# Kernel optimization log

Hardware: AMD Instinct MI355X
Metric: run time of the kernel (lower is better)

Reference implementation:

```python
import jax, jax.numpy as jnp
import numpy as np

N, D, H, DEG = 20000, 128, 128, 32


def setup_inputs() -> dict:
    key = jax.random.key(0)
    ks = jax.random.split(key, 6)
    s = 0.02
    h = jax.random.normal(ks[0], (N, D), dtype=jnp.float32)
    # per-node neighbor indices, sorted by index (permutation invariance per docstring)
    nbr_idx = jnp.sort(jax.random.randint(ks[1], (N, DEG), 0, N), axis=-1)
    W_ih = jax.random.normal(ks[2], (4 * H, D), dtype=jnp.float32) * s
    W_hh = jax.random.normal(ks[3], (4 * H, H), dtype=jnp.float32) * s
    b_ih = jnp.zeros((4 * H,), jnp.float32)
    b_hh = jnp.zeros((4 * H,), jnp.float32)
    W_out = jax.random.normal(ks[4], (H, D + H), dtype=jnp.float32) * s
    b_out = jnp.zeros((H,), jnp.float32)
    return {"h": h, "nbr_idx": nbr_idx, "W_ih": W_ih, "W_hh": W_hh,
            "b_ih": b_ih, "b_hh": b_hh, "W_out": W_out, "b_out": b_out}


def reference(h, nbr_idx, W_ih, W_hh, b_ih, b_hh, W_out, b_out):
    # Gather neighbor features: [N, DEG, D]
    nbr = h[nbr_idx]
    # Precompute input-to-gate projections for all steps: [N, DEG, 4H]
    xg = jnp.einsum('ndi,gi->ndg', nbr, W_ih) + b_ih + b_hh
    xg = jnp.swapaxes(xg, 0, 1)  # [DEG, N, 4H] for scan over neighbor sequence
    h0 = jnp.zeros((h.shape[0], W_hh.shape[1]), h.dtype)
    c0 = jnp.zeros_like(h0)

    def step(carry, g_t):
        hp, cp = carry
        g = g_t + hp @ W_hh.T            # [N, 4H]
        i, f, gg, o = jnp.split(g, 4, axis=-1)  # PyTorch gate order i,f,g,o
        c = jax.nn.sigmoid(f) * cp + jax.nn.sigmoid(i) * jnp.tanh(gg)
        hn = jax.nn.sigmoid(o) * jnp.tanh(c)
        return (hn, c), None

    (agg, _), _ = jax.lax.scan(step, (h0, c0), xg)  # agg = final hidden state [N, H]
    combined = jnp.concatenate([h, agg], axis=-1)   # [N, D+H]
    return jax.nn.relu(combined @ W_out.T + b_out)  # [N, H]
```

## Files before the change

kernel.cpp:

```cpp
#include <hip/hip_runtime.h>

#define NN 20000
#define DD 128
#define HH 128
#define G4 512
#define DEG 32
#define NPB 48
#define NBLK 417

typedef __attribute__((ext_vector_type(4))) float f32x4;
typedef __attribute__((ext_vector_type(8))) short s16x8;

#ifndef __has_builtin
#define __has_builtin(x) 0
#endif

static __device__ __forceinline__ float fexp2(float x){
#if __has_builtin(__builtin_amdgcn_exp2f)
  return __builtin_amdgcn_exp2f(x);
#else
  return exp2f(x);
#endif
}
static __device__ __forceinline__ float frcp(float x){
#if __has_builtin(__builtin_amdgcn_rcpf)
  return __builtin_amdgcn_rcpf(x);
#else
  return 1.f/x;
#endif
}

static __device__ __forceinline__ unsigned cvt_pk_bf16(float lo, float hi){
  unsigned r;
  asm("v_cvt_pk_bf16_f32 %0, %1, %2" : "=v"(r) : "v"(lo), "v"(hi));
  return r;
}
static __device__ __forceinline__ s16x8 ld8bf(const float* __restrict__ p){
  f32x4 a = *(const f32x4*)p;
  f32x4 b = *(const f32x4*)(p+4);
  union{unsigned u[4]; s16x8 v;} z;
  z.u[0]=cvt_pk_bf16(a[0],a[1]);
  z.u[1]=cvt_pk_bf16(a[2],a[3]);
  z.u[2]=cvt_pk_bf16(b[0],b[1]);
  z.u[3]=cvt_pk_bf16(b[2],b[3]);
  return z.v;
}
static __device__ __forceinline__ s16x8 ld8bf_s(const float* __restrict__ p, float s){
  f32x4 a = *(const f32x4*)p;
  f32x4 b = *(const f32x4*)(p+4);
  union{unsigned u[4]; s16x8 v;} z;
  z.u[0]=cvt_pk_bf16(a[0]*s,a[1]*s);
  z.u[1]=cvt_pk_bf16(a[2]*s,a[3]*s);
  z.u[2]=cvt_pk_bf16(b[0]*s,b[1]*s);
  z.u[3]=cvt_pk_bf16(b[2]*s,b[3]*s);
  return z.v;
}
static __device__ __forceinline__ float lo16f(unsigned u){
  union{unsigned x; float f;} v; v.x = u << 16; return v.f;
}
static __device__ __forceinline__ float hi16f(unsigned u){
  union{unsigned x; float f;} v; v.x = u & 0xffff0000u; return v.f;
}
#define NLOG2E -1.44269504f
#define TLOG2E  2.88539008f

__global__ __launch_bounds__(512,2) void k_hp(
    const float* __restrict__ h, const float* __restrict__ W_ih,
    const float* __restrict__ b_ih, const float* __restrict__ b_hh,
    unsigned short* __restrict__ Hp)
{
  const int tid=threadIdx.x, w=tid>>6, lane=tid&63, lo=lane&15, hi=lane>>4;
  const float SC[4]={NLOG2E,NLOG2E,TLOG2E,NLOG2E};
  s16x8 A[4][4];
#pragma unroll
  for(int g=0;g<4;++g){
    const float* wr=W_ih+(size_t)(128*g+16*w+lo)*DD+8*hi;
#pragma unroll
    for(int c=0;c<4;++c) A[g][c]=ld8bf_s(wr+32*c, SC[g]);
  }
  f32x4 bb[4];
#pragma unroll
  for(int g=0;g<4;++g){
    const int gcb=128*g+16*w+4*hi;
    bb[g]=(*(const f32x4*)(b_ih+gcb) + *(const f32x4*)(b_hh+gcb))*SC[g];
  }
  const int nchunk = (blockIdx.x < 57) ? 2 : 1;
  for(int cc=0; cc<nchunk; ++cc){
    const int n0 = ((cc? 256+blockIdx.x : blockIdx.x))*64;
    f32x4 acc[4][4];
#pragma unroll
    for(int g=0;g<4;++g)
#pragma unroll
      for(int nt=0;nt<4;++nt) acc[g][nt]=(f32x4)0.f;
#pragma unroll
    for(int c=0;c<4;++c){
      s16x8 B[4];
#pragma unroll
      for(int nt=0;nt<4;++nt){
        int nd=n0+16*nt+lo; if(nd>=NN) nd=NN-1;
        B[nt]=ld8bf(h+(size_t)nd*DD+32*c+8*hi);
      }
#pragma unroll
      for(int g=0;g<4;++g)
#pragma unroll
        for(int nt=0;nt<4;++nt)
          acc[g][nt]=__builtin_amdgcn_mfma_f32_16x16x32_bf16(A[g][c],B[nt],acc[g][nt],0,0,0);
    }
#pragma unroll
    for(int nt=0;nt<4;++nt){
      int nd=n0+16*nt+lo;
      if(nd<NN){
        unsigned short* p = Hp + (size_t)nd*G4 + w*64 + hi*16;
        uint4 q0, q1;
        q0.x=cvt_pk_bf16(acc[0][nt][0]+bb[0][0], acc[0][nt][1]+bb[0][1]);
        q0.y=cvt_pk_bf16(acc[0][nt][2]+bb[0][2], acc[0][nt][3]+bb[0][3]);
        q0.z=cvt_pk_bf16(acc[1][nt][0]+bb[1][0], acc[1][nt][1]+bb[1][1]);
        q0.w=cvt_pk_bf16(acc[1][nt][2]+bb[1][2], acc[1][nt][3]+bb[1][3]);
        q1.x=cvt_pk_bf16(acc[2][nt][0]+bb[2][0], acc[2][nt][1]+bb[2][1]);
        q1.y=cvt_pk_bf16(acc[2][nt][2]+bb[2][2], acc[2][nt][3]+bb[2][3]);
        q1.z=cvt_pk_bf16(acc[3][nt][0]+bb[3][0], acc[3][nt][1]+bb[3][1]);
        q1.w=cvt_pk_bf16(acc[3][nt][2]+bb[3][2], acc[3][nt][3]+bb[3][3]);
        *(uint4*)p = q0;
        *(uint4*)(p+8) = q1;
      }
    }
  }
}

static __device__ __forceinline__ void unpack_acc(const uint4 q[2], f32x4 acc[4]){
  acc[0][0]=lo16f(q[0].x); acc[0][1]=hi16f(q[0].x); acc[0][2]=lo16f(q[0].y); acc[0][3]=hi16f(q[0].y);
  acc[1][0]=lo16f(q[0].z); acc[1][1]=hi16f(q[0].z); acc[1][2]=lo16f(q[0].w); acc[1][3]=hi16f(q[0].w);
  acc[2][0]=lo16f(q[1].x); acc[2][1]=hi16f(q[1].x); acc[2][2]=lo16f(q[1].y); acc[2][3]=hi16f(q[1].y);
  acc[3][0]=lo16f(q[1].z); acc[3][1]=hi16f(q[1].z); acc[3][2]=lo16f(q[1].w); acc[3][3]=hi16f(q[1].w);
}

static __device__ __forceinline__ void cell_update(const f32x4 acc[4], float C[4],
                                                   char* wb, int waddr){
  float hv[4];
#pragma unroll
  for(int r=0;r<4;++r){
    float ei=fexp2(acc[0][r]);
    float ef=fexp2(acc[1][r]);
    float eg=fexp2(acc[2][r]);
    float eo=fexp2(acc[3][r]);
    float itgT=__builtin_fmaf(eg, TLOG2E, -TLOG2E)*frcp((1.f+ei)*(1.f+eg));
    float Cn=__builtin_fmaf(C[r], frcp(1.f+ef), itgT);
    C[r]=Cn;
    float ec=fexp2(Cn);
    hv[r]=(ec-1.f)*frcp((1.f+eo)*(1.f+ec));
  }
  uint2 pk;
  pk.x=cvt_pk_bf16(hv[0],hv[1]);
  pk.y=cvt_pk_bf16(hv[2],hv[3]);
  *(uint2*)(wb + waddr) = pk;
}

__global__ __launch_bounds__(512,1) void k_lstm(
    const float* __restrict__ h, const int* __restrict__ nbr,
    const float* __restrict__ W_hh, const unsigned short* __restrict__ Hp,
    const float* __restrict__ W_out, const float* __restrict__ b_out,
    float* __restrict__ out)
{
  __shared__ unsigned short hpd[3][2][16*HH];
  __shared__ int nlds[DEG*NPB];
  const int tid=threadIdx.x, w=tid>>6, lane=tid&63, lo=lane&15, hi=lane>>4;
  const int n0=blockIdx.x*NPB;
  const int swz=(lo&7)<<4;
  const int woff=w*64+hi*16;
  const int waddr=((lo*256 + 32*w + 8*hi) ^ swz);
  const float SC[4]={NLOG2E,NLOG2E,TLOG2E,NLOG2E};

  s16x8 A[4][4];
#pragma unroll
  for(int g=0;g<4;++g){
    const float* wr=W_hh+(size_t)(128*g+16*w+lo)*HH+8*hi;
#pragma unroll
    for(int c=0;c<4;++c) A[g][c]=ld8bf_s(wr+32*c, SC[g]);
  }
  {
#pragma unroll
    for(int g=0;g<3;++g){
      unsigned* z=(unsigned*)&hpd[g][0][0];
      z[tid]=0u; z[tid+512]=0u;
    }
#pragma unroll
    for(int i=0;i<3;++i){
      int idx=tid+512*i;
      int node=idx>>5;
      int src=n0+node; if(src>=NN) src=NN-1;
      nlds[(idx&31)*NPB + node] = nbr[src*DEG + (idx&31)]*G4;
    }
  }
  __syncthreads();

  float cst[3][4]={{0.f,0.f,0.f,0.f},{0.f,0.f,0.f,0.f},{0.f,0.f,0.f,0.f}};

  uint4 qA[2], qB[2], qC[2];
  {
    const unsigned short* gp=Hp+(size_t)nlds[lo]+woff;
    qA[0]=*(const uint4*)gp; qA[1]=*(const uint4*)(gp+8);
  }

#define PHASE(g, QUSE, QLOAD, LOFF) { \
    { const unsigned short* gp_=Hp+(size_t)nlds[LOFF]+woff; \
      QLOAD[0]=*(const uint4*)gp_; QLOAD[1]=*(const uint4*)(gp_+8); } \
    s16x8 Bg[4]; \
    const char* rb_=(const char*)&hpd[g][t&1][0]; \
    _Pragma("unroll") \
    for(int c=0;c<4;++c) Bg[c]=*(const s16x8*)(rb_ + (((lo*256 + 64*c + 16*hi)) ^ swz)); \
    f32x4 acc_[4]; \
    unpack_acc(QUSE, acc_); \
    _Pragma("unroll") \
    for(int c=0;c<4;++c) \
      _Pragma("unroll") \
      for(int gg=0;gg<4;++gg) \
        acc_[gg]=__builtin_amdgcn_mfma_f32_16x16x32_bf16(A[gg][c],Bg[c],acc_[gg],0,0,0); \
    cell_update(acc_, cst[g], (char*)&hpd[g][(t+1)&1][0], waddr); }

  for(int t=0;t<DEG;++t){
    const int tn=(t+1<DEG)? t+1 : t;
    PHASE(0, qA, qB, t*NPB + 16 + lo)
    PHASE(1, qB, qC, t*NPB + 32 + lo)
    PHASE(2, qC, qA, tn*NPB + lo)
    asm volatile("s_waitcnt lgkmcnt(0)\n\ts_barrier" ::: "memory");
  }
#undef PHASE

  s16x8 AO[8];
  {
    const float* wr=W_out+(size_t)(16*w+lo)*256+8*hi;
#pragma unroll
    for(int c=0;c<8;++c) AO[c]=ld8bf(wr+32*c);
  }
  const int ob=16*w+4*hi;
  f32x4 bias=*(const f32x4*)(b_out+ob);
#pragma unroll
  for(int g=0;g<3;++g){
    const int node=n0+g*16+lo;
    const int nc = (node<NN)? node : NN-1;
    s16x8 BB[8];
    const float* hr=h+(size_t)nc*DD+8*hi;
#pragma unroll
    for(int c=0;c<4;++c) BB[c]=ld8bf(hr+32*c);
    const char* rb=(const char*)&hpd[g][0][0];
#pragma unroll
    for(int c=0;c<4;++c)
      BB[4+c]=*(const s16x8*)(rb + (((lo*256 + 64*c + 16*hi)) ^ swz));
    f32x4 acc=(f32x4)0.f;
#pragma unroll
    for(int c=0;c<8;++c) acc=__builtin_amdgcn_mfma_f32_16x16x32_bf16(AO[c],BB[c],acc,0,0,0);
#pragma unroll
    for(int r=0;r<4;++r){ float v=acc[r]+bias[r]; acc[r]=v>0.f?v:0.f; }
    if(node<NN) *(f32x4*)(out+(size_t)node*HH+ob)=acc;
  }
}

extern "C" void kernel_launch(void* const* d_in, const int* in_sizes, int n_in,
                              void* d_out, int out_size, void* d_ws, size_t ws_size,
                              hipStream_t stream)
{
  const float* h     = (const float*)d_in[0];
  const int*   nbr   = (const int*)d_in[1];
  const float* W_ih  = (const float*)d_in[2];
  const float* W_hh  = (const float*)d_in[3];
  const float* b_ih  = (const float*)d_in[4];
  const float* b_hh  = (const float*)d_in[5];
  const float* W_out = (const float*)d_in[6];
  const float* b_out = (const float*)d_in[7];
  unsigned short* Hp = (unsigned short*)d_ws;

  k_hp<<<256, 512, 0, stream>>>(h, W_ih, b_ih, b_hh, Hp);
  k_lstm<<<NBLK, 512, 0, stream>>>(h, nbr, W_hh, Hp, W_out, b_out, (float*)d_out);
}
```

Baseline: 212.0 us.

## Use persistent LSTM blocks with atomic work queue over 32-node tiles

The recurrence kernel now processes 32 nodes per tile (two 16-node groups) instead of 48, launches a fixed grid of 512 persistent blocks at two blocks per CU, and pulls further tiles from a global atomic counter that the first kernel resets. This aims to fix the tail imbalance of 417 one-shot blocks and raise occupancy so more waves hide latency. In exchange, each wave has less interleaving of independent recurrences to cover MFMA and gather latency, and each tile pays an extra barrier plus an atomic. The counter reset depends on the first kernel running before the second on the same stream.

```diff
diff --git a/kernel.cpp b/kernel.cpp
--- a/kernel.cpp
+++ b/kernel.cpp
@@ -5,8 +5,9 @@
 #define HH 128
 #define G4 512
 #define DEG 32
-#define NPB 48
-#define NBLK 417
+#define NPB 32
+#define PAIRS 625
+#define GRID2 512
 
 typedef __attribute__((ext_vector_type(4))) float f32x4;
 typedef __attribute__((ext_vector_type(8))) short s16x8;
@@ -14,6 +15,8 @@
 #ifndef __has_builtin
 #define __has_builtin(x) 0
 #endif
+
+__device__ int g_cnt;
 
 static __device__ __forceinline__ float fexp2(float x){
 #if __has_builtin(__builtin_amdgcn_exp2f)
@@ -69,6 +72,7 @@
     const float* __restrict__ b_ih, const float* __restrict__ b_hh,
     unsigned short* __restrict__ Hp)
 {
+  if(blockIdx.x==0 && threadIdx.x==0) g_cnt = GRID2;
   const int tid=threadIdx.x, w=tid>>6, lane=tid&63, lo=lane&15, hi=lane>>4;
   const float SC[4]={NLOG2E,NLOG2E,TLOG2E,NLOG2E};
   s16x8 A[4][4];
@@ -155,16 +159,16 @@
   *(uint2*)(wb + waddr) = pk;
 }
 
-__global__ __launch_bounds__(512,1) void k_lstm(
+__global__ __launch_bounds__(512,2) void k_lstm(
     const float* __restrict__ h, const int* __restrict__ nbr,
     const float* __restrict__ W_hh, const unsigned short* __restrict__ Hp,
     const float* __restrict__ W_out, const float* __restrict__ b_out,
     float* __restrict__ out)
 {
-  __shared__ unsigned short hpd[3][2][16*HH];
+  __shared__ unsigned short hpd[2][2][16*HH];
   __shared__ int nlds[DEG*NPB];
+  __shared__ int spair;
   const int tid=threadIdx.x, w=tid>>6, lane=tid&63, lo=lane&15, hi=lane>>4;
-  const int n0=blockIdx.x*NPB;
   const int swz=(lo&7)<<4;
   const int woff=w*64+hi*16;
   const int waddr=((lo*256 + 32*w + 8*hi) ^ swz);
@@ -177,29 +181,31 @@
 #pragma unroll
     for(int c=0;c<4;++c) A[g][c]=ld8bf_s(wr+32*c, SC[g]);
   }
-  {
-#pragma unroll
-    for(int g=0;g<3;++g){
-      unsigned* z=(unsigned*)&hpd[g][0][0];
-      z[tid]=0u; z[tid+512]=0u;
-    }
-#pragma unroll
-    for(int i=0;i<3;++i){
-      int idx=tid+512*i;
-      int node=idx>>5;
-      int src=n0+node; if(src>=NN) src=NN-1;
-      nlds[(idx&31)*NPB + node] = nbr[src*DEG + (idx&31)]*G4;
-    }
-  }
-  __syncthreads();
-
-  float cst[3][4]={{0.f,0.f,0.f,0.f},{0.f,0.f,0.f,0.f},{0.f,0.f,0.f,0.f}};
-
-  uint4 qA[2], qB[2], qC[2];
-  {
-    const unsigned short* gp=Hp+(size_t)nlds[lo]+woff;
-    qA[0]=*(const uint4*)gp; qA[1]=*(const uint4*)(gp+8);
-  }
+
+  int pair = blockIdx.x;
+  for(;;){
+    const int n0 = pair*NPB;
+    {
+#pragma unroll
+      for(int g=0;g<2;++g){
+        unsigned* z=(unsigned*)&hpd[g][0][0];
+        z[tid]=0u; z[tid+512]=0u;
+      }
+#pragma unroll
+      for(int i=0;i<2;++i){
+        int idx=tid+512*i;
+        nlds[(idx&31)*NPB + (idx>>5)] = nbr[n0*DEG + idx]*G4;
+      }
+    }
+    __syncthreads();
+
+    float cst[2][4]={{0.f,0.f,0.f,0.f},{0.f,0.f,0.f,0.f}};
+
+    uint4 qA[2], qB[2];
+    {
+      const unsigned short* gp=Hp+(size_t)nlds[lo]+woff;
+      qA[0]=*(const uint4*)gp; qA[1]=*(const uint4*)(gp+8);
+    }
 
 #define PHASE(g, QUSE, QLOAD, LOFF) { \
     { const unsigned short* gp_=Hp+(size_t)nlds[LOFF]+woff; \
@@ -217,41 +223,45 @@
         acc_[gg]=__builtin_amdgcn_mfma_f32_16x16x32_bf16(A[gg][c],Bg[c],acc_[gg],0,0,0); \
     cell_update(acc_, cst[g], (char*)&hpd[g][(t+1)&1][0], waddr); }
 
-  for(int t=0;t<DEG;++t){
-    const int tn=(t+1<DEG)? t+1 : t;
-    PHASE(0, qA, qB, t*NPB + 16 + lo)
-    PHASE(1, qB, qC, t*NPB + 32 + lo)
-    PHASE(2, qC, qA, tn*NPB + lo)
-    asm volatile("s_waitcnt lgkmcnt(0)\n\ts_barrier" ::: "memory");
-  }
+    for(int t=0;t<DEG;++t){
+      const int tn=(t+1<DEG)? t+1 : t;
+      PHASE(0, qA, qB, t*NPB + 16 + lo)
+      PHASE(1, qB, qA, tn*NPB + lo)
+      asm volatile("s_waitcnt lgkmcnt(0)\n\ts_barrier" ::: "memory");
+    }
 #undef PHASE
 
-  s16x8 AO[8];
-  {
-    const float* wr=W_out+(size_t)(16*w+lo)*256+8*hi;
-#pragma unroll
-    for(int c=0;c<8;++c) AO[c]=ld8bf(wr+32*c);
-  }
-  const int ob=16*w+4*hi;
-  f32x4 bias=*(const f32x4*)(b_out+ob);
-#pragma unroll
-  for(int g=0;g<3;++g){
-    const int node=n0+g*16+lo;
-    const int nc = (node<NN)? node : NN-1;
-    s16x8 BB[8];
-    const float* hr=h+(size_t)nc*DD+8*hi;
-#pragma unroll
-    for(int c=0;c<4;++c) BB[c]=ld8bf(hr+32*c);
-    const char* rb=(const char*)&hpd[g][0][0];
-#pragma unroll
-    for(int c=0;c<4;++c)
-      BB[4+c]=*(const s16x8*)(rb + (((lo*256 + 64*c + 16*hi)) ^ swz));
-    f32x4 acc=(f32x4)0.f;
-#pragma unroll
-    for(int c=0;c<8;++c) acc=__builtin_amdgcn_mfma_f32_16x16x32_bf16(AO[c],BB[c],acc,0,0,0);
-#pragma unroll
-    for(int r=0;r<4;++r){ float v=acc[r]+bias[r]; acc[r]=v>0.f?v:0.f; }
-    if(node<NN) *(f32x4*)(out+(size_t)node*HH+ob)=acc;
+    s16x8 AO[8];
+    {
+      const float* wr=W_out+(size_t)(16*w+lo)*256+8*hi;
+#pragma unroll
+      for(int c=0;c<8;++c) AO[c]=ld8bf(wr+32*c);
+    }
+    const int ob=16*w+4*hi;
+    f32x4 bias=*(const f32x4*)(b_out+ob);
+#pragma unroll
+    for(int g=0;g<2;++g){
+      const int node=n0+g*16+lo;
+      s16x8 BB[8];
+      const float* hr=h+(size_t)node*DD+8*hi;
+#pragma unroll
+      for(int c=0;c<4;++c) BB[c]=ld8bf(hr+32*c);
+      const char* rb=(const char*)&hpd[g][0][0];
+#pragma unroll
+      for(int c=0;c<4;++c)
+        BB[4+c]=*(const s16x8*)(rb + (((lo*256 + 64*c + 16*hi)) ^ swz));
+      f32x4 acc=(f32x4)0.f;
+#pragma unroll
+      for(int c=0;c<8;++c) acc=__builtin_amdgcn_mfma_f32_16x16x32_bf16(AO[c],BB[c],acc,0,0,0);
+#pragma unroll
+      for(int r=0;r<4;++r){ float v=acc[r]+bias[r]; acc[r]=v>0.f?v:0.f; }
+      *(f32x4*)(out+(size_t)node*HH+ob)=acc;
+    }
+
+    if(tid==0) spair = atomicAdd(&g_cnt, 1);
+    __syncthreads();
+    pair = spair;
+    if(pair >= PAIRS) break;
   }
 }
 
@@ -270,5 +280,5 @@
   unsigned short* Hp = (unsigned short*)d_ws;
 
   k_hp<<<256, 512, 0, stream>>>(h, W_ih, b_ih, b_hh, Hp);
-  k_lstm<<<NBLK, 512, 0, stream>>>(h, nbr, W_hh, Hp, W_out, b_out, (float*)d_out);
-}
+  k_lstm<<<GRID2, 512, 0, stream>>>(h, nbr, W_hh, Hp, W_out, b_out, (float*)d_out);
+}
```

New measurement: 208.9 us. Within noise of the previous version (-1.4%).

## Give each wave its own 16-node group with W_hh shared in LDS

Applied to the files above, without the earlier changes.

The LSTM scan is restructured so each wavefront independently processes a 16-node group across all 32 steps. The full bf16 W_hh now sits in 160KB dynamic LDS, and each wave keeps its hidden state in a private LDS region. This removes the per-step block-wide barrier and the 8-wave cooperative gate split of the old kernel. The trade-off is more LDS traffic for A fragments (re-read every MFMA), 32 cell-state registers per lane, and W_out loaded per wave from global memory. With 256 blocks of 8 waves covering 1250 groups, some waves sit idle and occupancy is limited by the large LDS allocation.

```diff
diff --git a/kernel.cpp b/kernel.cpp
--- a/kernel.cpp
+++ b/kernel.cpp
@@ -5,8 +5,7 @@
 #define HH 128
 #define G4 512
 #define DEG 32
-#define NPB 48
-#define NBLK 417
+#define NG 1250
 
 typedef __attribute__((ext_vector_type(4))) float f32x4;
 typedef __attribute__((ext_vector_type(8))) short s16x8;
@@ -127,131 +126,139 @@
   }
 }
 
-static __device__ __forceinline__ void unpack_acc(const uint4 q[2], f32x4 acc[4]){
-  acc[0][0]=lo16f(q[0].x); acc[0][1]=hi16f(q[0].x); acc[0][2]=lo16f(q[0].y); acc[0][3]=hi16f(q[0].y);
-  acc[1][0]=lo16f(q[0].z); acc[1][1]=hi16f(q[0].z); acc[1][2]=lo16f(q[0].w); acc[1][3]=hi16f(q[0].w);
-  acc[2][0]=lo16f(q[1].x); acc[2][1]=hi16f(q[1].x); acc[2][2]=lo16f(q[1].y); acc[2][3]=hi16f(q[1].y);
-  acc[3][0]=lo16f(q[1].z); acc[3][1]=hi16f(q[1].z); acc[3][2]=lo16f(q[1].w); acc[3][3]=hi16f(q[1].w);
-}
-
-static __device__ __forceinline__ void cell_update(const f32x4 acc[4], float C[4],
-                                                   char* wb, int waddr){
-  float hv[4];
-#pragma unroll
-  for(int r=0;r<4;++r){
-    float ei=fexp2(acc[0][r]);
-    float ef=fexp2(acc[1][r]);
-    float eg=fexp2(acc[2][r]);
-    float eo=fexp2(acc[3][r]);
-    float itgT=__builtin_fmaf(eg, TLOG2E, -TLOG2E)*frcp((1.f+ei)*(1.f+eg));
-    float Cn=__builtin_fmaf(C[r], frcp(1.f+ef), itgT);
-    C[r]=Cn;
-    float ec=fexp2(Cn);
-    hv[r]=(ec-1.f)*frcp((1.f+eo)*(1.f+ec));
-  }
-  uint2 pk;
-  pk.x=cvt_pk_bf16(hv[0],hv[1]);
-  pk.y=cvt_pk_bf16(hv[2],hv[3]);
-  *(uint2*)(wb + waddr) = pk;
-}
-
-__global__ __launch_bounds__(512,1) void k_lstm(
+__global__ __launch_bounds__(512,1) void k_scan(
     const float* __restrict__ h, const int* __restrict__ nbr,
     const float* __restrict__ W_hh, const unsigned short* __restrict__ Hp,
     const float* __restrict__ W_out, const float* __restrict__ b_out,
     float* __restrict__ out)
 {
-  __shared__ unsigned short hpd[3][2][16*HH];
-  __shared__ int nlds[DEG*NPB];
+  extern __shared__ char smem[];
   const int tid=threadIdx.x, w=tid>>6, lane=tid&63, lo=lane&15, hi=lane>>4;
-  const int n0=blockIdx.x*NPB;
+
+  {
+    const int r=tid;
+    const float s = ((r>>7)==2) ? TLOG2E : NLOG2E;
+    const float* wr = W_hh + (size_t)r*HH;
+    const int sw = (r&7)<<4;
+#pragma unroll
+    for(int j=0;j<16;++j){
+      s16x8 v = ld8bf_s(wr + 8*j, s);
+      *(s16x8*)(smem + ((r*256 + j*16) ^ sw)) = v;
+    }
+  }
+  __syncthreads();
+
+  const int grp = w*256 + blockIdx.x;
+  if(grp >= NG) return;
+  const int n0 = grp*16;
+
   const int swz=(lo&7)<<4;
-  const int woff=w*64+hi*16;
-  const int waddr=((lo*256 + 32*w + 8*hi) ^ swz);
-  const float SC[4]={NLOG2E,NLOG2E,TLOG2E,NLOG2E};
-
-  s16x8 A[4][4];
-#pragma unroll
-  for(int g=0;g<4;++g){
-    const float* wr=W_hh+(size_t)(128*g+16*w+lo)*HH+8*hi;
-#pragma unroll
-    for(int c=0;c<4;++c) A[g][c]=ld8bf_s(wr+32*c, SC[g]);
-  }
-  {
-#pragma unroll
-    for(int g=0;g<3;++g){
-      unsigned* z=(unsigned*)&hpd[g][0][0];
-      z[tid]=0u; z[tid+512]=0u;
-    }
-#pragma unroll
-    for(int i=0;i<3;++i){
-      int idx=tid+512*i;
-      int node=idx>>5;
-      int src=n0+node; if(src>=NN) src=NN-1;
-      nlds[(idx&31)*NPB + node] = nbr[src*DEG + (idx&31)]*G4;
-    }
-  }
-  __syncthreads();
-
-  float cst[3][4]={{0.f,0.f,0.f,0.f},{0.f,0.f,0.f,0.f},{0.f,0.f,0.f,0.f}};
-
-  uint4 qA[2], qB[2], qC[2];
-  {
-    const unsigned short* gp=Hp+(size_t)nlds[lo]+woff;
-    qA[0]=*(const uint4*)gp; qA[1]=*(const uint4*)(gp+8);
-  }
-
-#define PHASE(g, QUSE, QLOAD, LOFF) { \
-    { const unsigned short* gp_=Hp+(size_t)nlds[LOFF]+woff; \
-      QLOAD[0]=*(const uint4*)gp_; QLOAD[1]=*(const uint4*)(gp_+8); } \
-    s16x8 Bg[4]; \
-    const char* rb_=(const char*)&hpd[g][t&1][0]; \
-    _Pragma("unroll") \
-    for(int c=0;c<4;++c) Bg[c]=*(const s16x8*)(rb_ + (((lo*256 + 64*c + 16*hi)) ^ swz)); \
-    f32x4 acc_[4]; \
-    unpack_acc(QUSE, acc_); \
-    _Pragma("unroll") \
-    for(int c=0;c<4;++c) \
-      _Pragma("unroll") \
-      for(int gg=0;gg<4;++gg) \
-        acc_[gg]=__builtin_amdgcn_mfma_f32_16x16x32_bf16(A[gg][c],Bg[c],acc_[gg],0,0,0); \
-    cell_update(acc_, cst[g], (char*)&hpd[g][(t+1)&1][0], waddr); }
-
+  char* hreg = smem + 131072 + w*4096;
+  const char* rdA[4]; const char* rdB[4];
+#pragma unroll
+  for(int c=0;c<4;++c){
+    const int off = (lo*256 + 64*c + 16*hi) ^ swz;
+    rdA[c] = smem + off;
+    rdB[c] = hreg + off;
+  }
+#pragma unroll
+  for(int i=0;i<4;++i){
+    uint4 z4={0u,0u,0u,0u};
+    *(uint4*)(hreg + lane*16 + i*1024) = z4;
+  }
+
+  float cst[32];
+#pragma unroll
+  for(int i=0;i<32;++i) cst[i]=0.f;
+
+  const int* nbp = nbr + (size_t)(n0 + lo)*DEG;
+  int idx_cur = nbp[0];
+
+#pragma unroll 1
   for(int t=0;t<DEG;++t){
-    const int tn=(t+1<DEG)? t+1 : t;
-    PHASE(0, qA, qB, t*NPB + 16 + lo)
-    PHASE(1, qB, qC, t*NPB + 32 + lo)
-    PHASE(2, qC, qA, tn*NPB + lo)
-    asm volatile("s_waitcnt lgkmcnt(0)\n\ts_barrier" ::: "memory");
-  }
-#undef PHASE
-
-  s16x8 AO[8];
-  {
-    const float* wr=W_out+(size_t)(16*w+lo)*256+8*hi;
-#pragma unroll
-    for(int c=0;c<8;++c) AO[c]=ld8bf(wr+32*c);
-  }
-  const int ob=16*w+4*hi;
-  f32x4 bias=*(const f32x4*)(b_out+ob);
-#pragma unroll
-  for(int g=0;g<3;++g){
-    const int node=n0+g*16+lo;
-    const int nc = (node<NN)? node : NN-1;
-    s16x8 BB[8];
-    const float* hr=h+(size_t)nc*DD+8*hi;
-#pragma unroll
-    for(int c=0;c<4;++c) BB[c]=ld8bf(hr+32*c);
-    const char* rb=(const char*)&hpd[g][0][0];
-#pragma unroll
-    for(int c=0;c<4;++c)
-      BB[4+c]=*(const s16x8*)(rb + (((lo*256 + 64*c + 16*hi)) ^ swz));
-    f32x4 acc=(f32x4)0.f;
-#pragma unroll
-    for(int c=0;c<8;++c) acc=__builtin_amdgcn_mfma_f32_16x16x32_bf16(AO[c],BB[c],acc,0,0,0);
-#pragma unroll
-    for(int r=0;r<4;++r){ float v=acc[r]+bias[r]; acc[r]=v>0.f?v:0.f; }
-    if(node<NN) *(f32x4*)(out+(size_t)node*HH+ob)=acc;
+    int tn=(t+1<DEG)? t+1 : t;
+    int idx_next = nbp[tn];
+    const char* gp = (const char*)Hp + (size_t)(unsigned)idx_cur*1024 + hi*32;
+    uint4 q[16];
+#pragma unroll
+    for(int db=0;db<8;++db){
+      q[2*db  ]=*(const uint4*)(gp + db*128);
+      q[2*db+1]=*(const uint4*)(gp + db*128 + 16);
+    }
+    s16x8 B[4];
+#pragma unroll
+    for(int c=0;c<4;++c) B[c]=*(const s16x8*)(rdB[c]);
+
+#pragma unroll
+    for(int half=0;half<2;++half){
+      f32x4 acc[4][4];
+#pragma unroll
+      for(int g=0;g<4;++g)
+#pragma unroll
+        for(int dl=0;dl<4;++dl){
+          const uint4& a=q[2*(dl+4*half)];
+          const uint4& b=q[2*(dl+4*half)+1];
+          if(g==0){ acc[0][dl][0]=lo16f(a.x); acc[0][dl][1]=hi16f(a.x); acc[0][dl][2]=lo16f(a.y); acc[0][dl][3]=hi16f(a.y); }
+          if(g==1){ acc[1][dl][0]=lo16f(a.z); acc[1][dl][1]=hi16f(a.z); acc[1][dl][2]=lo16f(a.w); acc[1][dl][3]=hi16f(a.w); }
+          if(g==2){ acc[2][dl][0]=lo16f(b.x); acc[2][dl][1]=hi16f(b.x); acc[2][dl][2]=lo16f(b.y); acc[2][dl][3]=hi16f(b.y); }
+          if(g==3){ acc[3][dl][0]=lo16f(b.z); acc[3][dl][1]=hi16f(b.z); acc[3][dl][2]=lo16f(b.w); acc[3][dl][3]=hi16f(b.w); }
+        }
+#pragma unroll
+      for(int c=0;c<4;++c)
+#pragma unroll
+        for(int g=0;g<4;++g)
+#pragma unroll
+          for(int dl=0;dl<4;++dl){
+            const int m = g*8 + dl + 4*half;
+            s16x8 Af = *(const s16x8*)(rdA[c] + m*4096);
+            acc[g][dl]=__builtin_amdgcn_mfma_f32_16x16x32_bf16(Af,B[c],acc[g][dl],0,0,0);
+          }
+#pragma unroll
+      for(int dl=0;dl<4;++dl){
+        const int db = dl + 4*half;
+        float hv[4];
+#pragma unroll
+        for(int r=0;r<4;++r){
+          float ei=fexp2(acc[0][dl][r]);
+          float ef=fexp2(acc[1][dl][r]);
+          float eg=fexp2(acc[2][dl][r]);
+          float eo=fexp2(acc[3][dl][r]);
+          float itgT=__builtin_fmaf(eg, TLOG2E, -TLOG2E)*frcp((1.f+ei)*(1.f+eg));
+          float Cn=__builtin_fmaf(cst[db*4+r], frcp(1.f+ef), itgT);
+          cst[db*4+r]=Cn;
+          float ec=fexp2(Cn);
+          hv[r]=(ec-1.f)*frcp((1.f+eo)*(1.f+ec));
+        }
+        uint2 pk;
+        pk.x=cvt_pk_bf16(hv[0],hv[1]);
+        pk.y=cvt_pk_bf16(hv[2],hv[3]);
+        *(uint2*)(hreg + ((lo*256 + 32*db + 8*hi) ^ swz)) = pk;
+      }
+    }
+    idx_cur = idx_next;
+  }
+
+  s16x8 BB[8];
+#pragma unroll
+  for(int c=0;c<4;++c) BB[c]=ld8bf(h + (size_t)(n0+lo)*DD + 32*c + 8*hi);
+#pragma unroll
+  for(int c=0;c<4;++c) BB[4+c]=*(const s16x8*)(rdB[c]);
+  f32x4 po[8];
+#pragma unroll
+  for(int m=0;m<8;++m) po[m]=(f32x4)0.f;
+#pragma unroll
+  for(int m=0;m<8;++m)
+#pragma unroll
+    for(int c=0;c<8;++c){
+      s16x8 Af=ld8bf(W_out + (size_t)(16*m+lo)*256 + 32*c + 8*hi);
+      po[m]=__builtin_amdgcn_mfma_f32_16x16x32_bf16(Af,BB[c],po[m],0,0,0);
+    }
+#pragma unroll
+  for(int m=0;m<8;++m){
+    f32x4 bias=*(const f32x4*)(b_out + 16*m + 4*hi);
+#pragma unroll
+    for(int r=0;r<4;++r){ float v=po[m][r]+bias[r]; po[m][r]=v>0.f?v:0.f; }
+    *(f32x4*)(out + (size_t)(n0+lo)*HH + 16*m + 4*hi)=po[m];
   }
 }
 
@@ -270,5 +277,5 @@
   unsigned short* Hp = (unsigned short*)d_ws;
 
   k_hp<<<256, 512, 0, stream>>>(h, W_ih, b_ih, b_hh, Hp);
-  k_lstm<<<NBLK, 512, 0, stream>>>(h, nbr, W_hh, Hp, W_out, b_out, (float*)d_out);
-}
+  k_scan<<<256, 512, 163840, stream>>>(h, nbr, W_hh, Hp, W_out, b_out, (float*)d_out);
+}
```

Measured after the change: 264.9 us. 25.0% more time.
